# Kernel tuning notes

Hardware: AMD Instinct MI355X
Metric: run time of the kernel (lower is better)

## Reference

```python
import jax, jax.numpy as jnp
import numpy as np

D_OUT, D_IN, R, N_TOK = 4096, 4096, 16, 8192

def setup_inputs() -> dict:
    key = jax.random.key(0)
    k1, k2, k3, k4 = jax.random.split(key, 4)
    x = jax.random.normal(k1, (N_TOK, D_IN), dtype=jnp.float32)
    W = jax.random.normal(k2, (D_OUT, D_IN), dtype=jnp.float32) * (1.0 / np.sqrt(D_IN))
    bias = jax.random.normal(k3, (D_OUT,), dtype=jnp.float32) * 0.02
    lora_B = jnp.zeros((D_OUT, R), dtype=jnp.float32)  # torch init: zeros
    lora_A = jax.random.normal(k4, (R, D_IN), dtype=jnp.float32) / R  # torch init: randn / r
    lora_scale = jnp.float32(1.0)
    return {"x": x, "W": W, "bias": bias, "lora_B": lora_B, "lora_A": lora_A, "lora_scale": lora_scale}

def reference(x, W, bias, lora_B, lora_A, lora_scale):
    # Faithful to torch: weight = W + scale * B @ A; out = x @ weight.T + bias
    weight = W + lora_scale * (lora_B @ lora_A)  # [d_out, d_in]
    return jnp.einsum('ni,oi->no', x, weight) + bias
```

## Files before the change

kernel.cpp:

```cpp
#include <hip/hip_runtime.h>
#include <stdint.h>
#include <stddef.h>

#define M_TOK 8192
#define N_OUT 4096
#define K_IN  4096
#define R_LORA 16

#define BM 256
#define BN 256
#define BK 64
#define NT (K_IN / BK)

#define WEFF_BLOCKS ((K_IN / 1024) * (N_OUT / 32))
#define CAST_BLOCKS ((M_TOK * K_IN) / (8 * 256))

typedef __bf16 bf16_t;
typedef __bf16 bf16x4 __attribute__((ext_vector_type(4)));
typedef __bf16 bf16x8 __attribute__((ext_vector_type(8)));
typedef float floatx4 __attribute__((ext_vector_type(4)));

__device__ inline void async_copy16(const bf16_t* g, bf16_t* l) {
  __builtin_amdgcn_global_load_lds(
      (__attribute__((address_space(1))) void*)(uintptr_t)(const void*)g,
      (__attribute__((address_space(3))) void*)l,
      16, 0, 0);
}

#define BAR()   __builtin_amdgcn_s_barrier()
#define VMCNT4  asm volatile("s_waitcnt vmcnt(4)" ::: "memory")
#define VMCNT2  asm volatile("s_waitcnt vmcnt(2)" ::: "memory")
#define VMCNT0  asm volatile("s_waitcnt vmcnt(0)" ::: "memory")
#define LGKM0   asm volatile("s_waitcnt lgkmcnt(0)" ::: "memory")

__global__ __launch_bounds__(256) void prep_fused(
    const float* __restrict__ x, bf16_t* __restrict__ xb,
    const float* __restrict__ W, const float* __restrict__ lB,
    const float* __restrict__ lA, const float* __restrict__ scale_p,
    bf16_t* __restrict__ wb) {
  const int b = blockIdx.x;
  if (b < WEFF_BLOCKS) {
    const int kbase = (b & 3) * 1024 + threadIdx.x * 4;
    const int o0    = (b >> 2) * 32;
    const float scale = *scale_p;

    float4 areg[R_LORA];
#pragma unroll
    for (int r = 0; r < R_LORA; ++r)
      areg[r] = *(const float4*)(lA + (size_t)r * K_IN + kbase);

    for (int oo = 0; oo < 32; ++oo) {
      const int o = o0 + oo;
      float4 w = *(const float4*)(W + (size_t)o * K_IN + kbase);
      float a0 = w.x, a1 = w.y, a2 = w.z, a3 = w.w;
#pragma unroll
      for (int r = 0; r < R_LORA; ++r) {
        float bb = lB[(size_t)o * R_LORA + r] * scale;
        a0 += bb * areg[r].x; a1 += bb * areg[r].y;
        a2 += bb * areg[r].z; a3 += bb * areg[r].w;
      }
      bf16x4 v;
      v[0] = (bf16_t)a0; v[1] = (bf16_t)a1; v[2] = (bf16_t)a2; v[3] = (bf16_t)a3;
      *(bf16x4*)(wb + (size_t)o * K_IN + kbase) = v;
    }
  } else {
    const size_t t = (size_t)(b - WEFF_BLOCKS) * 256 + threadIdx.x;
    const float4* xp = (const float4*)x + t * 2;
    float4 a0 = xp[0];
    float4 a1 = xp[1];
    bf16x8 v;
    v[0] = (bf16_t)a0.x; v[1] = (bf16_t)a0.y; v[2] = (bf16_t)a0.z; v[3] = (bf16_t)a0.w;
    v[4] = (bf16_t)a1.x; v[5] = (bf16_t)a1.y; v[6] = (bf16_t)a1.z; v[7] = (bf16_t)a1.w;
    *(bf16x8*)(xb + t * 8) = v;
  }
}

__global__ __launch_bounds__(512, 2) void gemm_bt256(const bf16_t* __restrict__ A,
                                                     const bf16_t* __restrict__ Bw,
                                                     const float* __restrict__ bias,
                                                     float* __restrict__ C) {
  __shared__ bf16_t sA[2 * 2 * 128 * 64];
  __shared__ bf16_t sB[2 * 2 * 128 * 64];

  const int tid  = threadIdx.x;
  const int wave = tid >> 6;
  const int lane = tid & 63;
  const int lr   = lane & 15;
  const int quad = lane >> 4;
  const int wr   = wave >> 2;
  const int wc   = wave & 3;

  const int bid = blockIdx.x;
  const int swz = (bid & 7) * 64 + (bid >> 3);
  const int bn  = (swz & 15) * BN;
  const int bm  = (swz >> 4) * BM;

  const int t8  = tid >> 3;
  const int col = ((tid & 7) ^ (t8 & 7)) * 8;
  const bf16_t* pA00 = A + (size_t)(bm +   0 + t8) * K_IN + col;
  const bf16_t* pA01 = A + (size_t)(bm + 128 + t8) * K_IN + col;
  const bf16_t* pA10 = A + (size_t)(bm +  64 + t8) * K_IN + col;
  const bf16_t* pA11 = A + (size_t)(bm + 192 + t8) * K_IN + col;
  const int brl = (t8 >> 5) * 64 + (t8 & 31);
  const bf16_t* pB00 = Bw + (size_t)(bn +   0 + brl +  0) * K_IN + col;
  const bf16_t* pB01 = Bw + (size_t)(bn + 128 + brl +  0) * K_IN + col;
  const bf16_t* pB10 = Bw + (size_t)(bn +   0 + brl + 32) * K_IN + col;
  const bf16_t* pB11 = Bw + (size_t)(bn + 128 + brl + 32) * K_IN + col;

  const char* aR0 = (const char*)sA + (size_t)(wr * 64 + lr) * 128 + ((quad) ^ (lr & 7)) * 16;
  const char* aR1 = (const char*)sA + (size_t)(wr * 64 + lr) * 128 + ((4 + quad) ^ (lr & 7)) * 16;
  const char* bR0 = (const char*)sB + (size_t)(wc * 32 + lr) * 128 + ((quad) ^ (lr & 7)) * 16;
  const char* bR1 = (const char*)sB + (size_t)(wc * 32 + lr) * 128 + ((4 + quad) ^ (lr & 7)) * 16;

  floatx4 acc[8][4];
#pragma unroll
  for (int m = 0; m < 8; ++m)
#pragma unroll
    for (int n = 0; n < 4; ++n) acc[m][n] = {0.f, 0.f, 0.f, 0.f};

#define STAGE_A0(nb) do { \
    async_copy16(pA00, sA + (nb)         + wave * 512); \
    async_copy16(pA01, sA + (nb) + 4096  + wave * 512); \
    pA00 += BK; pA01 += BK; } while (0)
#define STAGE_A1(nb) do { \
    async_copy16(pA10, sA + (nb) + 8192  + wave * 512); \
    async_copy16(pA11, sA + (nb) + 12288 + wave * 512); \
    pA10 += BK; pA11 += BK; } while (0)
#define STAGE_B0(nb) do { \
    async_copy16(pB00, sB + (nb)         + wave * 512); \
    async_copy16(pB01, sB + (nb) + 4096  + wave * 512); \
    pB00 += BK; pB01 += BK; } while (0)
#define STAGE_B1(nb) do { \
    async_copy16(pB10, sB + (nb) + 8192  + wave * 512); \
    async_copy16(pB11, sB + (nb) + 12288 + wave * 512); \
    pB10 += BK; pB11 += BK; } while (0)

#define READ_A(mh) do { _Pragma("unroll") for (int mm = 0; mm < 4; ++mm) { \
    a[mm][0] = *(const bf16x8*)(aR0 + bufofs + (mh) * 16384 + mm * 2048); \
    a[mm][1] = *(const bf16x8*)(aR1 + bufofs + (mh) * 16384 + mm * 2048); } } while (0)
#define READ_B(nh) do { _Pragma("unroll") for (int nn = 0; nn < 2; ++nn) { \
    b[(nh) * 2 + nn][0] = *(const bf16x8*)(bR0 + bufofs + (nh) * 16384 + nn * 2048); \
    b[(nh) * 2 + nn][1] = *(const bf16x8*)(bR1 + bufofs + (nh) * 16384 + nn * 2048); } } while (0)

#define MFMA_QUAD(mh, nh) do { \
    __builtin_amdgcn_s_setprio(1); \
    _Pragma("unroll") for (int mm = 0; mm < 4; ++mm) \
    _Pragma("unroll") for (int nn = 0; nn < 2; ++nn) { \
      acc[(mh)*4+mm][(nh)*2+nn] = __builtin_amdgcn_mfma_f32_16x16x32_bf16( \
          a[mm][0], b[(nh)*2+nn][0], acc[(mh)*4+mm][(nh)*2+nn], 0, 0, 0); \
      acc[(mh)*4+mm][(nh)*2+nn] = __builtin_amdgcn_mfma_f32_16x16x32_bf16( \
          a[mm][1], b[(nh)*2+nn][1], acc[(mh)*4+mm][(nh)*2+nn], 0, 0, 0); } \
    __builtin_amdgcn_s_setprio(0); } while (0)

  STAGE_A0(0);
  STAGE_B0(0);
  STAGE_B1(0);
  STAGE_A1(0);
  VMCNT4;
  BAR();

  int bufofs = 0;
  for (int t = 0; t < NT; ++t) {
    const int nb = ((t + 1) & 1) * 16384;
    const bool st = (t + 1 < NT);
    bf16x8 a[4][2], b[4][2];

    READ_A(0);
    READ_B(0);
    if (st) { STAGE_A0(nb); VMCNT4; } else { VMCNT2; }
    BAR(); LGKM0;
    MFMA_QUAD(0, 0);
    BAR();

    READ_B(1);
    if (st) { STAGE_B0(nb); VMCNT4; } else { VMCNT0; }
    BAR(); LGKM0;
    MFMA_QUAD(0, 1);
    BAR();

    READ_A(1);
    if (st) STAGE_B1(nb);
    BAR(); LGKM0;
    MFMA_QUAD(1, 1);
    BAR();

    if (st) { STAGE_A1(nb); VMCNT4; }
    BAR(); LGKM0;
    MFMA_QUAD(1, 0);
    BAR();

    bufofs ^= 32768;
  }
#undef STAGE_A0
#undef STAGE_A1
#undef STAGE_B0
#undef STAGE_B1
#undef READ_A
#undef READ_B
#undef MFMA_QUAD

#pragma unroll
  for (int n = 0; n < 4; ++n) {
    const int colc = bn + wc * 64 + n * 16 + lr;
    const float bb = bias[colc];
#pragma unroll
    for (int m = 0; m < 8; ++m) {
      const int row0 = bm + wr * 128 + m * 16 + quad * 4;
      floatx4 v = acc[m][n];
#pragma unroll
      for (int r = 0; r < 4; ++r)
        C[(size_t)(row0 + r) * N_OUT + colc] = v[r] + bb;
    }
  }
}

__global__ __launch_bounds__(256) void lora_xa(const float* __restrict__ x,
                                               const float* __restrict__ lA,
                                               const float* __restrict__ scale_p,
                                               float* __restrict__ t) {
  int m = blockIdx.x;
  int r = threadIdx.x & 15;
  int kcn = threadIdx.x >> 4;
  float acc = 0.f;
  const float* xr = x + (size_t)m * K_IN + kcn * 256;
  const float* ar = lA + (size_t)r * K_IN + kcn * 256;
  for (int k = 0; k < 256; k += 4) {
    float4 xv = *(const float4*)(xr + k);
    float4 av = *(const float4*)(ar + k);
    acc += xv.x * av.x + xv.y * av.y + xv.z * av.z + xv.w * av.w;
  }
  __shared__ float s[256];
  s[threadIdx.x] = acc;
  __syncthreads();
  if (threadIdx.x < 16) {
    float v = 0.f;
    for (int i = 0; i < 16; ++i) v += s[threadIdx.x + i * 16];
    t[(size_t)m * 16 + threadIdx.x] = v * (*scale_p);
  }
}

__global__ __launch_bounds__(256) void gemm_f32_fb(const float* __restrict__ X,
                                                   const float* __restrict__ W,
                                                   const float* __restrict__ bias,
                                                   const float* __restrict__ t,
                                                   const float* __restrict__ lB,
                                                   float* __restrict__ C) {
  __shared__ float sX[64][17];
  __shared__ float sW[64][17];
  int tid = threadIdx.x;
  int tx = tid & 15, ty = tid >> 4;
  int m0 = blockIdx.y * 64, n0 = blockIdx.x * 64;
  int lrow = tid >> 2, lcol = (tid & 3) * 4;
  float acc[4][4] = {};
  for (int k0 = 0; k0 < K_IN; k0 += 16) {
    __syncthreads();
    float4 xv = *(const float4*)(X + (size_t)(m0 + lrow) * K_IN + k0 + lcol);
    float4 wv = *(const float4*)(W + (size_t)(n0 + lrow) * K_IN + k0 + lcol);
    sX[lrow][lcol + 0] = xv.x; sX[lrow][lcol + 1] = xv.y;
    sX[lrow][lcol + 2] = xv.z; sX[lrow][lcol + 3] = xv.w;
    sW[lrow][lcol + 0] = wv.x; sW[lrow][lcol + 1] = wv.y;
    sW[lrow][lcol + 2] = wv.z; sW[lrow][lcol + 3] = wv.w;
    __syncthreads();
#pragma unroll
    for (int kk = 0; kk < 16; ++kk) {
      float xr[4], wr[4];
#pragma unroll
      for (int i = 0; i < 4; ++i) { xr[i] = sX[ty * 4 + i][kk]; wr[i] = sW[tx * 4 + i][kk]; }
#pragma unroll
      for (int i = 0; i < 4; ++i)
#pragma unroll
        for (int j = 0; j < 4; ++j) acc[i][j] += xr[i] * wr[j];
    }
  }
  for (int j = 0; j < 4; ++j) {
    int n = n0 + tx * 4 + j;
    float bb = bias[n];
    for (int i = 0; i < 4; ++i) {
      int m = m0 + ty * 4 + i;
      float l = 0.f;
      for (int r = 0; r < R_LORA; ++r) l += t[(size_t)m * 16 + r] * lB[(size_t)n * 16 + r];
      C[(size_t)m * N_OUT + n] = acc[i][j] + bb + l;
    }
  }
}

extern "C" void kernel_launch(void* const* d_in, const int* in_sizes, int n_in,
                              void* d_out, int out_size, void* d_ws, size_t ws_size,
                              hipStream_t stream) {
  const float* x     = (const float*)d_in[0];
  const float* W     = (const float*)d_in[1];
  const float* bias  = (const float*)d_in[2];
  const float* lB    = (const float*)d_in[3];
  const float* lA    = (const float*)d_in[4];
  const float* scale = (const float*)d_in[5];
  float* out = (float*)d_out;

  const size_t x_bytes = (size_t)M_TOK * K_IN * sizeof(bf16_t);
  const size_t w_bytes = (size_t)N_OUT * K_IN * sizeof(bf16_t);

  if (ws_size >= x_bytes + w_bytes) {
    bf16_t* xb = (bf16_t*)d_ws;
    bf16_t* wb = (bf16_t*)((char*)d_ws + x_bytes);
    prep_fused<<<WEFF_BLOCKS + CAST_BLOCKS, 256, 0, stream>>>(x, xb, W, lB, lA, scale, wb);
    gemm_bt256<<<(M_TOK / BM) * (N_OUT / BN), 512, 0, stream>>>(xb, wb, bias, out);
  } else {
    float* t = (float*)d_ws;
    lora_xa<<<M_TOK, 256, 0, stream>>>(x, lA, scale, t);
    gemm_f32_fb<<<dim3(N_OUT / 64, M_TOK / 64), 256, 0, stream>>>(x, W, bias, t, lB, out);
  }
}
```

Baseline: 566.1 us.

## Software-pipeline LDS fragment reads ahead of MFMAs and halve weight-prep block size

The GEMM main loop is unrolled by two buffers and restructured so LDS fragment reads for the next MFMA quadrant are issued before the current MFMAs, using separate register sets. This removes the explicit lgkmcnt waits and one barrier pair per step. The goal is to overlap LDS latency with matrix math and global-to-LDS copies. Separately, the LoRA weight-merge prep uses 16 output rows per block instead of 32, doubling the block count for more parallelism. The trade-off is higher register pressure and tighter vmcnt accounting, which risks races if the waits are wrong.

Result: slower. 718.1 us (+26.8%).

```diff
diff --git a/kernel.cpp b/kernel.cpp
--- a/kernel.cpp
+++ b/kernel.cpp
@@ -12,7 +12,7 @@
 #define BK 64
 #define NT (K_IN / BK)
 
-#define WEFF_BLOCKS ((K_IN / 1024) * (N_OUT / 32))
+#define WEFF_BLOCKS ((K_IN / 1024) * (N_OUT / 16))
 #define CAST_BLOCKS ((M_TOK * K_IN) / (8 * 256))
 
 typedef __bf16 bf16_t;
@@ -28,10 +28,8 @@
 }
 
 #define BAR()   __builtin_amdgcn_s_barrier()
-#define VMCNT4  asm volatile("s_waitcnt vmcnt(4)" ::: "memory")
 #define VMCNT2  asm volatile("s_waitcnt vmcnt(2)" ::: "memory")
 #define VMCNT0  asm volatile("s_waitcnt vmcnt(0)" ::: "memory")
-#define LGKM0   asm volatile("s_waitcnt lgkmcnt(0)" ::: "memory")
 
 __global__ __launch_bounds__(256) void prep_fused(
     const float* __restrict__ x, bf16_t* __restrict__ xb,
@@ -41,7 +39,7 @@
   const int b = blockIdx.x;
   if (b < WEFF_BLOCKS) {
     const int kbase = (b & 3) * 1024 + threadIdx.x * 4;
-    const int o0    = (b >> 2) * 32;
+    const int o0    = (b >> 2) * 16;
     const float scale = *scale_p;
 
     float4 areg[R_LORA];
@@ -49,7 +47,7 @@
     for (int r = 0; r < R_LORA; ++r)
       areg[r] = *(const float4*)(lA + (size_t)r * K_IN + kbase);
 
-    for (int oo = 0; oo < 32; ++oo) {
+    for (int oo = 0; oo < 16; ++oo) {
       const int o = o0 + oo;
       float4 w = *(const float4*)(W + (size_t)o * K_IN + kbase);
       float a0 = w.x, a1 = w.y, a2 = w.z, a3 = w.w;
@@ -118,6 +116,8 @@
 #pragma unroll
     for (int n = 0; n < 4; ++n) acc[m][n] = {0.f, 0.f, 0.f, 0.f};
 
+  bf16x8 a0[4][2], a1[4][2], bA[2][2], bB[2][2], bC[2][2];
+
 #define STAGE_A0(nb) do { \
     async_copy16(pA00, sA + (nb)         + wave * 512); \
     async_copy16(pA01, sA + (nb) + 4096  + wave * 512); \
@@ -135,69 +135,74 @@
     async_copy16(pB11, sB + (nb) + 12288 + wave * 512); \
     pB10 += BK; pB11 += BK; } while (0)
 
-#define READ_A(mh) do { _Pragma("unroll") for (int mm = 0; mm < 4; ++mm) { \
-    a[mm][0] = *(const bf16x8*)(aR0 + bufofs + (mh) * 16384 + mm * 2048); \
-    a[mm][1] = *(const bf16x8*)(aR1 + bufofs + (mh) * 16384 + mm * 2048); } } while (0)
-#define READ_B(nh) do { _Pragma("unroll") for (int nn = 0; nn < 2; ++nn) { \
-    b[(nh) * 2 + nn][0] = *(const bf16x8*)(bR0 + bufofs + (nh) * 16384 + nn * 2048); \
-    b[(nh) * 2 + nn][1] = *(const bf16x8*)(bR1 + bufofs + (nh) * 16384 + nn * 2048); } } while (0)
-
-#define MFMA_QUAD(mh, nh) do { \
+#define RD_A(dst, mh, bofs) do { _Pragma("unroll") for (int mm = 0; mm < 4; ++mm) { \
+    dst[mm][0] = *(const bf16x8*)(aR0 + (bofs) + (mh) * 16384 + mm * 2048); \
+    dst[mm][1] = *(const bf16x8*)(aR1 + (bofs) + (mh) * 16384 + mm * 2048); } } while (0)
+#define RD_B(dst, nh, bofs) do { _Pragma("unroll") for (int nn = 0; nn < 2; ++nn) { \
+    dst[nn][0] = *(const bf16x8*)(bR0 + (bofs) + (nh) * 16384 + nn * 2048); \
+    dst[nn][1] = *(const bf16x8*)(bR1 + (bofs) + (nh) * 16384 + nn * 2048); } } while (0)
+
+#define MM(aset, bset, mh, nh) do { \
     __builtin_amdgcn_s_setprio(1); \
     _Pragma("unroll") for (int mm = 0; mm < 4; ++mm) \
     _Pragma("unroll") for (int nn = 0; nn < 2; ++nn) { \
       acc[(mh)*4+mm][(nh)*2+nn] = __builtin_amdgcn_mfma_f32_16x16x32_bf16( \
-          a[mm][0], b[(nh)*2+nn][0], acc[(mh)*4+mm][(nh)*2+nn], 0, 0, 0); \
+          aset[mm][0], bset[nn][0], acc[(mh)*4+mm][(nh)*2+nn], 0, 0, 0); \
       acc[(mh)*4+mm][(nh)*2+nn] = __builtin_amdgcn_mfma_f32_16x16x32_bf16( \
-          a[mm][1], b[(nh)*2+nn][1], acc[(mh)*4+mm][(nh)*2+nn], 0, 0, 0); } \
+          aset[mm][1], bset[nn][1], acc[(mh)*4+mm][(nh)*2+nn], 0, 0, 0); } \
     __builtin_amdgcn_s_setprio(0); } while (0)
 
-  STAGE_A0(0);
-  STAGE_B0(0);
-  STAGE_B1(0);
-  STAGE_A1(0);
-  VMCNT4;
+  STAGE_A0(0); STAGE_B0(0); STAGE_B1(0); STAGE_A1(0);
+  VMCNT2;
   BAR();
-
-  int bufofs = 0;
-  for (int t = 0; t < NT; ++t) {
-    const int nb = ((t + 1) & 1) * 16384;
-    const bool st = (t + 1 < NT);
-    bf16x8 a[4][2], b[4][2];
-
-    READ_A(0);
-    READ_B(0);
-    if (st) { STAGE_A0(nb); VMCNT4; } else { VMCNT2; }
-    BAR(); LGKM0;
-    MFMA_QUAD(0, 0);
-    BAR();
-
-    READ_B(1);
-    if (st) { STAGE_B0(nb); VMCNT4; } else { VMCNT0; }
-    BAR(); LGKM0;
-    MFMA_QUAD(0, 1);
-    BAR();
-
-    READ_A(1);
-    if (st) STAGE_B1(nb);
-    BAR(); LGKM0;
-    MFMA_QUAD(1, 1);
-    BAR();
-
-    if (st) { STAGE_A1(nb); VMCNT4; }
-    BAR(); LGKM0;
-    MFMA_QUAD(1, 0);
-    BAR();
-
-    bufofs ^= 32768;
+  RD_A(a0, 0, 0);
+  RD_B(bA, 0, 0);
+
+  for (int t = 0; t < NT; t += 2) {
+    const bool last = (t + 2 >= NT);
+
+    RD_B(bB, 1, 0);
+    STAGE_A0(16384);
+    MM(a0, bA, 0, 0);
+    VMCNT2; BAR();
+    RD_A(a1, 1, 0);
+    STAGE_B0(16384);
+    MM(a0, bB, 0, 1);
+    BAR();
+    STAGE_B1(16384);
+    MM(a1, bB, 1, 1);
+    VMCNT2; BAR();
+    STAGE_A1(16384);
+    MM(a1, bA, 1, 0);
+    RD_A(a0, 0, 32768);
+    RD_B(bC, 0, 32768);
+    VMCNT2; BAR();
+
+    RD_B(bB, 1, 32768);
+    if (!last) STAGE_A0(0);
+    MM(a0, bC, 0, 0);
+    if (last) { VMCNT0; } else { VMCNT2; }
+    BAR();
+    RD_A(a1, 1, 32768);
+    if (!last) STAGE_B0(0);
+    MM(a0, bB, 0, 1);
+    BAR();
+    if (!last) STAGE_B1(0);
+    MM(a1, bB, 1, 1);
+    if (!last) VMCNT2;
+    BAR();
+    if (!last) STAGE_A1(0);
+    MM(a1, bC, 1, 0);
+    if (!last) { RD_A(a0, 0, 0); RD_B(bA, 0, 0); VMCNT2; }
+    BAR();
   }
 #undef STAGE_A0
 #undef STAGE_A1
 #undef STAGE_B0
 #undef STAGE_B1
-#undef READ_A
-#undef READ_B
-#undef MFMA_QUAD
+#undef RD_A
+#undef RD_B
+#undef MM
 
 #pragma unroll
   for (int n = 0; n < 4; ++n) {
```
